# Kernel tuning notes

Hardware: AMD Instinct MI355X
Metric: run time of the kernel (lower is better)

## Reference

```python
import jax, jax.numpy as jnp
import numpy as np

N = 8192
IN_F = 256
OUT_F = 128
ALPHA = 0.2
NEG = -9000000000000000.0

def setup_inputs() -> dict:
    key = jax.random.key(0)
    k1, k2, k3, k4 = jax.random.split(key, 4)
    h = jax.random.normal(k1, (N, IN_F), dtype=jnp.float32)
    adj = jax.random.randint(k2, (N, N), 0, 2, dtype=jnp.int32)
    # xavier-uniform-like params
    limW = float(np.sqrt(6.0 / (IN_F + OUT_F)))
    W = jax.random.uniform(k3, (IN_F, OUT_F), minval=-limW, maxval=limW, dtype=jnp.float32)
    lima = float(np.sqrt(6.0 / (2 * OUT_F + 1)))
    a = jax.random.uniform(k4, (2 * OUT_F, 1), minval=-lima, maxval=lima, dtype=jnp.float32)
    return {"h": h, "adj": adj, "W": W, "a": a}

def reference(h, adj, W, a):
    Wh = h @ W  # [N, F]
    # e_ij = LeakyReLU(a1.Wh_i + a2.Wh_j) -- avoids [N,N,2F] intermediate
    a1 = a[:OUT_F, 0]  # [F]
    a2 = a[OUT_F:, 0]  # [F]
    f1 = Wh @ a1  # [N]
    f2 = Wh @ a2  # [N]
    e = jax.nn.leaky_relu(f1[:, None] + f2[None, :], negative_slope=ALPHA)  # [N,N]
    att = jnp.where(adj > 0, e, jnp.float32(NEG))
    att = jax.nn.softmax(att, axis=1)
    h_prime = att @ Wh  # [N, F]
    return h_prime
```

## Files before the change

### kernel.cpp

```cpp
#include <hip/hip_runtime.h>
#include <hip/hip_bf16.h>

#define N    8192
#define INF  256
#define OUTF 128
#define ALPHA 0.2f
#define JS   8
#define NTS  (N / JS / 32)

typedef __attribute__((ext_vector_type(8))) short bf16x8;
typedef __attribute__((ext_vector_type(4))) float f32x4;

__device__ __forceinline__ unsigned short f2bf(float x) {
    union { float f; unsigned u; } v; v.f = x;
    unsigned r = v.u + 0x7fff + ((v.u >> 16) & 1);
    return (unsigned short)(r >> 16);
}

__device__ __forceinline__ void gll16(const void* g, void* l) {
    __builtin_amdgcn_global_load_lds(
        (const __attribute__((address_space(1))) unsigned*)g,
        (__attribute__((address_space(3))) unsigned*)l, 16, 0, 0);
}

__global__ __launch_bounds__(256) void k01_prep(
        const int* __restrict__ adj, unsigned* __restrict__ bits,
        const float* __restrict__ h, const float* __restrict__ W,
        const float* __restrict__ a,
        unsigned short* __restrict__ WhTb, float* __restrict__ f1, float* __restrict__ f2) {
    __shared__ float hs[8][INF];
    const int t = threadIdx.x;

    if (blockIdx.x >= 1024) {
        const int pb = blockIdx.x - 1024;
        const int w  = t >> 6;
        const int ln = t & 63;
        const size_t wi0 = ((size_t)pb * 4 + w) * 32;
        #pragma unroll 2
        for (int it = 0; it < 32; ++it) {
            const size_t base = (wi0 + it) * 256;
            int v0 = adj[base + ln];
            int v1 = adj[base + 64 + ln];
            int v2 = adj[base + 128 + ln];
            int v3 = adj[base + 192 + ln];
            unsigned long long b0 = __ballot(v0 > 0);
            unsigned long long b1 = __ballot(v1 > 0);
            unsigned long long b2 = __ballot(v2 > 0);
            unsigned long long b3 = __ballot(v3 > 0);
            if (ln < 8) {
                int c = ln >> 1;
                unsigned long long bb = (c == 0) ? b0 : (c == 1) ? b1 : (c == 2) ? b2 : b3;
                bits[(wi0 + it) * 8 + ln] = (unsigned)(bb >> ((ln & 1) * 32));
            }
        }
        return;
    }

    const int i0 = blockIdx.x * 8;
    #pragma unroll
    for (int u = 0; u < 2; ++u) {
        int idx = u * 256 + t;
        int r   = idx >> 6;
        int kq  = idx & 63;
        *(float4*)&hs[r][kq * 4] = *(const float4*)(h + (size_t)(i0 + r) * INF + kq * 4);
    }
    __syncthreads();

    const int rg = t >> 5;
    const int ct = t & 31;
    float acc[4] = {0.f, 0.f, 0.f, 0.f};

    #pragma unroll 8
    for (int k = 0; k < INF; ++k) {
        float4 wv = *(const float4*)(W + (size_t)k * OUTF + ct * 4);
        float  hx = hs[rg][k];
        acc[0] += hx * wv.x; acc[1] += hx * wv.y;
        acc[2] += hx * wv.z; acc[3] += hx * wv.w;
    }

    const int r0 = i0 + rg;
    const int jb = r0 >> 5;
    const int jo = r0 & 31;
    #pragma unroll
    for (int cc = 0; cc < 4; ++cc)
        WhTb[(size_t)jb * 4096 + (ct * 4 + cc) * 32 + jo] = f2bf(acc[cc]);

    const float4 a1v = *(const float4*)(a + ct * 4);
    const float4 a2v = *(const float4*)(a + OUTF + ct * 4);
    float p1 = acc[0]*a1v.x + acc[1]*a1v.y + acc[2]*a1v.z + acc[3]*a1v.w;
    float p2 = acc[0]*a2v.x + acc[1]*a2v.y + acc[2]*a2v.z + acc[3]*a2v.w;
    #pragma unroll
    for (int off = 16; off > 0; off >>= 1) {
        p1 += __shfl_down(p1, off, 32);
        p2 += __shfl_down(p2, off, 32);
    }
    if (ct == 0) { f1[r0] = p1; f2[r0] = p2; }
}

__device__ __forceinline__ float pbit(float f1r, float fv, unsigned byte_,
                                      int u, float& dsum) {
    float s = f1r + fv;
    float e = fmaxf(s, ALPHA * s);
    float p = (byte_ & (1u << u)) ? __expf(e) : 0.f;
    dsum += p;
    return p;
}

#define K2CMP(WORD, PH, SLOT, JT)                                            \
    {                                                                        \
        float4 F0_ = *(const float4*)&f2s[(JT) * 32 + quad * 8];             \
        float4 F1_ = *(const float4*)&f2s[(JT) * 32 + quad * 8 + 4];         \
        unsigned byte_ = ((WORD) >> (quad << 3)) & 0xffu;                    \
        float p0_ = pbit(f1r, F0_.x, byte_, 0, dsum);                        \
        float p1_ = pbit(f1r, F0_.y, byte_, 1, dsum);                        \
        float p2_ = pbit(f1r, F0_.z, byte_, 2, dsum);                        \
        float p3_ = pbit(f1r, F0_.w, byte_, 3, dsum);                        \
        float p4_ = pbit(f1r, F1_.x, byte_, 4, dsum);                        \
        float p5_ = pbit(f1r, F1_.y, byte_, 5, dsum);                        \
        float p6_ = pbit(f1r, F1_.z, byte_, 6, dsum);                        \
        float p7_ = pbit(f1r, F1_.w, byte_, 7, dsum);                        \
        union { __hip_bfloat162 hh[4]; bf16x8 v; } pk_;                      \
        pk_.hh[0] = __float22bfloat162_rn(make_float2(p0_, p1_));            \
        pk_.hh[1] = __float22bfloat162_rn(make_float2(p2_, p3_));            \
        pk_.hh[2] = __float22bfloat162_rn(make_float2(p4_, p5_));            \
        pk_.hh[3] = __float22bfloat162_rn(make_float2(p6_, p7_));            \
        bf16x8 afrag = pk_.v;                                                \
        const char* bb_ = (const char*)&bsm[PH][(SLOT) * 4096] + laneb2;     \
        bf16x8 b0_ = *(const bf16x8*)(bb_);                                  \
        bf16x8 b1_ = *(const bf16x8*)(bb_ + 1024);                           \
        bf16x8 b2_ = *(const bf16x8*)(bb_ + 2048);                           \
        bf16x8 b3_ = *(const bf16x8*)(bb_ + 3072);                           \
        bf16x8 b4_ = *(const bf16x8*)(bb_ + 4096);                           \
        bf16x8 b5_ = *(const bf16x8*)(bb_ + 5120);                           \
        bf16x8 b6_ = *(const bf16x8*)(bb_ + 6144);                           \
        bf16x8 b7_ = *(const bf16x8*)(bb_ + 7168);                           \
        acc0 = __builtin_amdgcn_mfma_f32_16x16x32_bf16(afrag, b0_, acc0, 0, 0, 0); \
        acc1 = __builtin_amdgcn_mfma_f32_16x16x32_bf16(afrag, b1_, acc1, 0, 0, 0); \
        acc2 = __builtin_amdgcn_mfma_f32_16x16x32_bf16(afrag, b2_, acc2, 0, 0, 0); \
        acc3 = __builtin_amdgcn_mfma_f32_16x16x32_bf16(afrag, b3_, acc3, 0, 0, 0); \
        acc4 = __builtin_amdgcn_mfma_f32_16x16x32_bf16(afrag, b4_, acc4, 0, 0, 0); \
        acc5 = __builtin_amdgcn_mfma_f32_16x16x32_bf16(afrag, b5_, acc5, 0, 0, 0); \
        acc6 = __builtin_amdgcn_mfma_f32_16x16x32_bf16(afrag, b6_, acc6, 0, 0, 0); \
        acc7 = __builtin_amdgcn_mfma_f32_16x16x32_bf16(afrag, b7_, acc7, 0, 0, 0); \
    }

#define K2PAIR(W0, W1, PH, JT)                                               \
    {                                                                        \
        if ((JT) + 2 < NTS) {                                                \
            const char* ws_ = (const char*)WhTb + (size_t)(tile0 + (JT) + 2) * 8192; \
            char* bd_ = (char*)&bsm[(PH) ^ 1][0];                            \
            gll16(ws_ + t * 16,         bd_ + wv * 1024);                    \
            gll16(ws_ + 4096 + t * 16,  bd_ + 4096 + wv * 1024);             \
            gll16(ws_ + 8192 + t * 16,  bd_ + 8192 + wv * 1024);             \
            gll16(ws_ + 12288 + t * 16, bd_ + 12288 + wv * 1024);            \
        }                                                                    \
        K2CMP(W0, PH, 0, JT)                                                 \
        K2CMP(W1, PH, 1, (JT) + 1)                                           \
        __syncthreads();                                                     \
    }

__global__ __launch_bounds__(256, 4) void k2_attn(
        const unsigned* __restrict__ bits, const unsigned short* __restrict__ WhTb,
        const float* __restrict__ f1, const float* __restrict__ f2,
        float* __restrict__ num, float* __restrict__ den) {
    __shared__ unsigned short bsm[2][8192];
    __shared__ float f2s[1024];

    const int t    = threadIdx.x;
    const int wv   = t >> 6;
    const int ln   = t & 63;
    const int m16  = ln & 15;
    const int quad = ln >> 4;
    const int i0   = blockIdx.x * 64;
    const int s    = blockIdx.y;
    const int row  = i0 + wv * 16 + m16;
    const int tile0 = s * NTS;
    const int j0    = s * (N / JS);
    const int laneb2 = (m16 * 32 + quad * 8) * 2;

    *(float4*)&f2s[t * 4] = *(const float4*)(f2 + j0 + t * 4);
    {
        const char* ws0 = (const char*)WhTb + (size_t)tile0 * 8192;
        char* bd = (char*)&bsm[0][0];
        gll16(ws0 + t * 16,         bd + wv * 1024);
        gll16(ws0 + 4096 + t * 16,  bd + 4096 + wv * 1024);
        gll16(ws0 + 8192 + t * 16,  bd + 8192 + wv * 1024);
        gll16(ws0 + 12288 + t * 16, bd + 12288 + wv * 1024);
    }

    const float f1r = f1[row];
    const uint4* brow = (const uint4*)(bits + (size_t)row * 256 + tile0);

    f32x4 acc0 = {0.f,0.f,0.f,0.f}, acc1 = {0.f,0.f,0.f,0.f};
    f32x4 acc2 = {0.f,0.f,0.f,0.f}, acc3 = {0.f,0.f,0.f,0.f};
    f32x4 acc4 = {0.f,0.f,0.f,0.f}, acc5 = {0.f,0.f,0.f,0.f};
    f32x4 acc6 = {0.f,0.f,0.f,0.f}, acc7 = {0.f,0.f,0.f,0.f};
    float dsum = 0.f;

    uint4 bwc = brow[0];
    __syncthreads();

    for (int g = 0; g < NTS / 4; ++g) {
        uint4 bwn = brow[(g + 1 < NTS / 4) ? g + 1 : g];
        const int jtb = g * 4;
        K2PAIR(bwc.x, bwc.y, 0, jtb)
        K2PAIR(bwc.z, bwc.w, 1, jtb + 2)
        bwc = bwn;
    }

    dsum += __shfl_xor(dsum, 16);
    dsum += __shfl_xor(dsum, 32);
    if (quad == 0) den[(size_t)s * N + row] = dsum;

    float* np = num + (size_t)s * N * OUTF;
    #pragma unroll
    for (int r = 0; r < 4; ++r) {
        const size_t orow = (size_t)(i0 + wv * 16 + quad * 4 + r) * OUTF;
        np[orow + 0 * 16 + m16] = acc0[r];
        np[orow + 1 * 16 + m16] = acc1[r];
        np[orow + 2 * 16 + m16] = acc2[r];
        np[orow + 3 * 16 + m16] = acc3[r];
        np[orow + 4 * 16 + m16] = acc4[r];
        np[orow + 5 * 16 + m16] = acc5[r];
        np[orow + 6 * 16 + m16] = acc6[r];
        np[orow + 7 * 16 + m16] = acc7[r];
    }
}

__global__ __launch_bounds__(256) void k3_combine(
        const float* __restrict__ num, const float* __restrict__ den,
        float* __restrict__ out) {
    const int idx = blockIdx.x * 256 + threadIdx.x;
    const int row = idx >> 5;
    const int c4  = (idx & 31) * 4;
    float4 ns = {0.f,0.f,0.f,0.f};
    float  ds = 0.f;
    #pragma unroll
    for (int s = 0; s < JS; ++s) {
        float4 nv = *(const float4*)(num + ((size_t)s * N + row) * OUTF + c4);
        ns.x += nv.x; ns.y += nv.y; ns.z += nv.z; ns.w += nv.w;
        ds += den[(size_t)s * N + row];
    }
    const float inv = 1.0f / ds;
    float4 o = {ns.x * inv, ns.y * inv, ns.z * inv, ns.w * inv};
    *(float4*)(out + (size_t)row * OUTF + c4) = o;
}

extern "C" void kernel_launch(void* const* d_in, const int* in_sizes, int n_in,
                              void* d_out, int out_size, void* d_ws, size_t ws_size,
                              hipStream_t stream) {
    const float* h   = (const float*)d_in[0];
    const int*   adj = (const int*)  d_in[1];
    const float* W   = (const float*)d_in[2];
    const float* a   = (const float*)d_in[3];
    float* out = (float*)d_out;

    unsigned short* WhTb = (unsigned short*)d_ws;
    float*    f1   = (float*)(WhTb + (size_t)N * OUTF);
    float*    f2   = f1 + N;
    float*    den  = f2 + N;
    unsigned* bits = (unsigned*)(den + (size_t)JS * N);
    float*    num  = (float*)(bits + (size_t)N * (N / 32));

    k01_prep  <<<1024 + 2048, 256, 0, stream>>>(adj, bits, h, W, a, WhTb, f1, f2);
    k2_attn   <<<dim3(N / 64, JS), 256, 0, stream>>>(bits, WhTb, f1, f2, num, den);
    k3_combine<<<(N * OUTF / 4) / 256, 256, 0, stream>>>(num, den, out);
}
```

Measured before the change: 439.1 us.

## Fuse split-K combine into attention kernel and shrink LDS double buffer

The separate combine kernel is removed. Each attention block increments a per-row-block atomic counter, and the last of the JS split blocks sums the partial numerators and denominators and writes the normalized output. The LDS staging buffer is halved to one 32-column tile per phase, with a barrier after every tile instead of every pair, and launch bounds are raised to 5 blocks per CU. This saves one kernel launch and the extra pass over num/den, and may raise occupancy. In exchange it doubles the number of barriers, shortens the prefetch distance, and adds a memset plus an atomic-based tail done by only a few blocks.

Result: slower. 571.1 us (+30.0%).

```diff
diff --git a/kernel.cpp b/kernel.cpp
--- a/kernel.cpp
+++ b/kernel.cpp
@@ -106,8 +106,14 @@
     return p;
 }
 
-#define K2CMP(WORD, PH, SLOT, JT)                                            \
+#define K2SUB(WORD, PH, JT)                                                  \
     {                                                                        \
+        if ((JT) + 1 < NTS) {                                                \
+            const char* ws_ = (const char*)WhTb + (size_t)(tile0 + (JT) + 1) * 8192; \
+            char* bd_ = (char*)&bsm[(PH) ^ 1][0];                            \
+            gll16(ws_ + t * 16,        bd_ + wv * 1024);                     \
+            gll16(ws_ + 4096 + t * 16, bd_ + 4096 + wv * 1024);              \
+        }                                                                    \
         float4 F0_ = *(const float4*)&f2s[(JT) * 32 + quad * 8];             \
         float4 F1_ = *(const float4*)&f2s[(JT) * 32 + quad * 8 + 4];         \
         unsigned byte_ = ((WORD) >> (quad << 3)) & 0xffu;                    \
@@ -125,7 +131,7 @@
         pk_.hh[2] = __float22bfloat162_rn(make_float2(p4_, p5_));            \
         pk_.hh[3] = __float22bfloat162_rn(make_float2(p6_, p7_));            \
         bf16x8 afrag = pk_.v;                                                \
-        const char* bb_ = (const char*)&bsm[PH][(SLOT) * 4096] + laneb2;     \
+        const char* bb_ = (const char*)&bsm[PH][0] + laneb2;                 \
         bf16x8 b0_ = *(const bf16x8*)(bb_);                                  \
         bf16x8 b1_ = *(const bf16x8*)(bb_ + 1024);                           \
         bf16x8 b2_ = *(const bf16x8*)(bb_ + 2048);                           \
@@ -142,29 +148,18 @@
         acc5 = __builtin_amdgcn_mfma_f32_16x16x32_bf16(afrag, b5_, acc5, 0, 0, 0); \
         acc6 = __builtin_amdgcn_mfma_f32_16x16x32_bf16(afrag, b6_, acc6, 0, 0, 0); \
         acc7 = __builtin_amdgcn_mfma_f32_16x16x32_bf16(afrag, b7_, acc7, 0, 0, 0); \
-    }
-
-#define K2PAIR(W0, W1, PH, JT)                                               \
-    {                                                                        \
-        if ((JT) + 2 < NTS) {                                                \
-            const char* ws_ = (const char*)WhTb + (size_t)(tile0 + (JT) + 2) * 8192; \
-            char* bd_ = (char*)&bsm[(PH) ^ 1][0];                            \
-            gll16(ws_ + t * 16,         bd_ + wv * 1024);                    \
-            gll16(ws_ + 4096 + t * 16,  bd_ + 4096 + wv * 1024);             \
-            gll16(ws_ + 8192 + t * 16,  bd_ + 8192 + wv * 1024);             \
-            gll16(ws_ + 12288 + t * 16, bd_ + 12288 + wv * 1024);            \
-        }                                                                    \
-        K2CMP(W0, PH, 0, JT)                                                 \
-        K2CMP(W1, PH, 1, (JT) + 1)                                           \
         __syncthreads();                                                     \
     }
 
-__global__ __launch_bounds__(256, 4) void k2_attn(
+__global__ __launch_bounds__(256, 5) void k2_attn(
         const unsigned* __restrict__ bits, const unsigned short* __restrict__ WhTb,
         const float* __restrict__ f1, const float* __restrict__ f2,
-        float* __restrict__ num, float* __restrict__ den) {
-    __shared__ unsigned short bsm[2][8192];
+        float* __restrict__ num, float* __restrict__ den,
+        unsigned* __restrict__ cnt, float* __restrict__ out) {
+    __shared__ unsigned short bsm[2][4096];
     __shared__ float f2s[1024];
+    __shared__ int   lastf;
+    __shared__ float dls[64];
 
     const int t    = threadIdx.x;
     const int wv   = t >> 6;
@@ -182,10 +177,8 @@
     {
         const char* ws0 = (const char*)WhTb + (size_t)tile0 * 8192;
         char* bd = (char*)&bsm[0][0];
-        gll16(ws0 + t * 16,         bd + wv * 1024);
-        gll16(ws0 + 4096 + t * 16,  bd + 4096 + wv * 1024);
-        gll16(ws0 + 8192 + t * 16,  bd + 8192 + wv * 1024);
-        gll16(ws0 + 12288 + t * 16, bd + 12288 + wv * 1024);
+        gll16(ws0 + t * 16,        bd + wv * 1024);
+        gll16(ws0 + 4096 + t * 16, bd + 4096 + wv * 1024);
     }
 
     const float f1r = f1[row];
@@ -203,8 +196,10 @@
     for (int g = 0; g < NTS / 4; ++g) {
         uint4 bwn = brow[(g + 1 < NTS / 4) ? g + 1 : g];
         const int jtb = g * 4;
-        K2PAIR(bwc.x, bwc.y, 0, jtb)
-        K2PAIR(bwc.z, bwc.w, 1, jtb + 2)
+        K2SUB(bwc.x, 0, jtb + 0)
+        K2SUB(bwc.y, 1, jtb + 1)
+        K2SUB(bwc.z, 0, jtb + 2)
+        K2SUB(bwc.w, 1, jtb + 3)
         bwc = bwn;
     }
 
@@ -225,25 +220,37 @@
         np[orow + 6 * 16 + m16] = acc6[r];
         np[orow + 7 * 16 + m16] = acc7[r];
     }
-}
-
-__global__ __launch_bounds__(256) void k3_combine(
-        const float* __restrict__ num, const float* __restrict__ den,
-        float* __restrict__ out) {
-    const int idx = blockIdx.x * 256 + threadIdx.x;
-    const int row = idx >> 5;
-    const int c4  = (idx & 31) * 4;
-    float4 ns = {0.f,0.f,0.f,0.f};
-    float  ds = 0.f;
-    #pragma unroll
-    for (int s = 0; s < JS; ++s) {
-        float4 nv = *(const float4*)(num + ((size_t)s * N + row) * OUTF + c4);
-        ns.x += nv.x; ns.y += nv.y; ns.z += nv.z; ns.w += nv.w;
-        ds += den[(size_t)s * N + row];
-    }
-    const float inv = 1.0f / ds;
-    float4 o = {ns.x * inv, ns.y * inv, ns.z * inv, ns.w * inv};
-    *(float4*)(out + (size_t)row * OUTF + c4) = o;
+
+    __threadfence();
+    __syncthreads();
+    if (t == 0) lastf = (atomicAdd(&cnt[blockIdx.x], 1u) == JS - 1);
+    __syncthreads();
+    if (!lastf) return;
+    __threadfence();
+
+    if (t < 64) {
+        float d = 0.f;
+        #pragma unroll
+        for (int s2 = 0; s2 < JS; ++s2) d += den[(size_t)s2 * N + i0 + t];
+        dls[t] = 1.0f / d;
+    }
+    __syncthreads();
+
+    #pragma unroll
+    for (int e = 0; e < 8; ++e) {
+        int idx = e * 256 + t;
+        int r   = idx >> 5;
+        int c4  = (idx & 31) * 4;
+        float4 ns = {0.f,0.f,0.f,0.f};
+        #pragma unroll
+        for (int s2 = 0; s2 < JS; ++s2) {
+            float4 v = *(const float4*)(num + ((size_t)s2 * N + i0 + r) * OUTF + c4);
+            ns.x += v.x; ns.y += v.y; ns.z += v.z; ns.w += v.w;
+        }
+        const float inv = dls[r];
+        float4 o = {ns.x * inv, ns.y * inv, ns.z * inv, ns.w * inv};
+        *(float4*)(out + (size_t)(i0 + r) * OUTF + c4) = o;
+    }
 }
 
 extern "C" void kernel_launch(void* const* d_in, const int* in_sizes, int n_in,
@@ -261,8 +268,9 @@
     float*    den  = f2 + N;
     unsigned* bits = (unsigned*)(den + (size_t)JS * N);
     float*    num  = (float*)(bits + (size_t)N * (N / 32));
-
-    k01_prep  <<<1024 + 2048, 256, 0, stream>>>(adj, bits, h, W, a, WhTb, f1, f2);
-    k2_attn   <<<dim3(N / 64, JS), 256, 0, stream>>>(bits, WhTb, f1, f2, num, den);
-    k3_combine<<<(N * OUTF / 4) / 256, 256, 0, stream>>>(num, den, out);
-}
+    unsigned* cnt  = (unsigned*)(num + (size_t)JS * N * OUTF);
+
+    hipMemsetAsync(cnt, 0, (N / 64) * sizeof(unsigned), stream);
+    k01_prep<<<1024 + 2048, 256, 0, stream>>>(adj, bits, h, W, a, WhTb, f1, f2);
+    k2_attn <<<dim3(N / 64, JS), 256, 0, stream>>>(bits, WhTb, f1, f2, num, den, cnt, out);
+}
```
